# Kernel optimization log

Hardware: AMD Instinct MI355X
Metric: run time of the kernel (lower is better)

The kernel has to match this reference:

```python
import jax, jax.numpy as jnp
import numpy as np

B, S, H, I, E, TOP_K = 2, 2048, 1024, 2048, 8, 2


def setup_inputs() -> dict:
    key = jax.random.key(0)
    k1, k2, k3, k4, k5 = jax.random.split(key, 5)
    scale_h = 1.0 / np.sqrt(H)
    scale_i = 1.0 / np.sqrt(I)
    return {
        "hidden_states": jax.random.normal(k1, (B, S, H), dtype=jnp.float32),
        "router_w": jax.random.normal(k2, (H, E), dtype=jnp.float32) * scale_h,
        "gate_w": jax.random.normal(k3, (E, H, I), dtype=jnp.float32) * scale_h,
        "up_w": jax.random.normal(k4, (E, H, I), dtype=jnp.float32) * scale_h,
        "out_w": jax.random.normal(k5, (E, I, H), dtype=jnp.float32) * scale_i,
    }


def reference(hidden_states, router_w, gate_w, up_w, out_w):
    b, s, h = hidden_states.shape
    x = hidden_states.reshape(-1, h)  # [T, H], T = B*S

    # Router: logits -> softmax -> top-k -> renormalize -> dense routing matrix
    router_logits = x @ router_w  # [T, E]
    router_probs = jax.nn.softmax(router_logits, axis=-1)
    top_p, top_i = jax.lax.top_k(router_probs, TOP_K)  # [T, K]
    top_p = top_p / jnp.sum(top_p, axis=-1, keepdims=True)
    one_hot = jax.nn.one_hot(top_i, E, dtype=top_p.dtype)  # [T, K, E]
    routing_full = jnp.sum(one_hot * top_p[..., None], axis=1)  # [T, E]
    routing_full = routing_full.T  # [E, T]

    # Dense all-expert FFN (SwiGLU), as in the original batched einsum form
    gate = jnp.einsum("th,ehm->etm", x, gate_w)  # [E, T, I]
    gate = jax.nn.silu(gate)
    intermediate = jnp.einsum("th,ehm->etm", x, up_w)  # [E, T, I]
    hidden = intermediate * gate
    expert_out = jnp.einsum("eti,eih->eth", hidden, out_w)  # [E, T, H]

    # Weighted combine over experts
    out = jnp.sum(expert_out * routing_full[:, :, None], axis=0)  # [T, H]
    out = out.reshape(b, s, h)
    return out, router_logits
```

## Files before the change

### kernel.cpp

```cpp
#include <hip/hip_runtime.h>
#include <hip/hip_bf16.h>
#include <stdint.h>

#define TT 4096
#define HH 1024
#define II 2048
#define EE 8
#define RB 16
#define NRB (TT / RB)
#define CSTRIDE 32

typedef short bf16x8 __attribute__((ext_vector_type(8)));
typedef float f32x4 __attribute__((ext_vector_type(4)));

__device__ __forceinline__ unsigned short f2bf(float f) {
  unsigned u = __float_as_uint(f);
  u += 0x7FFF + ((u >> 16) & 1);
  return (unsigned short)(u >> 16);
}

__device__ __forceinline__ void gl_lds16(const void* g, void* l) {
  auto gp = reinterpret_cast<const __attribute__((address_space(1))) unsigned int*>(
      reinterpret_cast<uintptr_t>(g));
  auto lp = reinterpret_cast<__attribute__((address_space(3))) unsigned int*>(
      reinterpret_cast<uintptr_t>(l));
  __builtin_amdgcn_global_load_lds(gp, lp, 16, 0, 0);
}

__device__ __forceinline__ void transpose_tile_wide(const float* __restrict__ in,
                                                    unsigned short* __restrict__ out,
                                                    int M, int N, int mB, int nB,
                                                    unsigned int* tl, int tid) {
  union F4 { float4 v; float f[4]; };
  int n4 = tid & 31;
  int mph = tid >> 5;
  F4 a[4], bq[4];
  const float* base = in + (size_t)mB * N + nB + n4 * 4;
#pragma unroll
  for (int it = 0; it < 4; ++it) {
    const float* p = base + (size_t)(2 * (mph + it * 8)) * N;
    a[it].v = *(const float4*)p;
    bq[it].v = *(const float4*)(p + N);
  }
#pragma unroll
  for (int it = 0; it < 4; ++it) {
    int mp = mph + it * 8;
#pragma unroll
    for (int i = 0; i < 4; ++i) {
      int n = n4 * 4 + i;
      unsigned v = (unsigned)f2bf(a[it].f[i]) | ((unsigned)f2bf(bq[it].f[i]) << 16);
      tl[n * 32 + ((mp + (n >> 2) + (n & 3)) & 31)] = v;
    }
  }
  __syncthreads();
  int md = tid & 7;
  int nr = tid >> 3;
#pragma unroll
  for (int it = 0; it < 4; ++it) {
    int n = nr + it * 32;
    int rot = (n >> 2) + (n & 3);
    unsigned vv[4];
#pragma unroll
    for (int k = 0; k < 4; ++k)
      vv[k] = tl[n * 32 + ((md * 4 + k + rot) & 31)];
    *(uint4*)(out + (size_t)(nB + n) * M + mB + md * 8) = make_uint4(vv[0], vv[1], vv[2], vv[3]);
  }
}

__global__ __launch_bounds__(256, 4)
void front_kernel(const float* __restrict__ x, const float* __restrict__ rw,
                  const float* __restrict__ gw, const float* __restrict__ uw,
                  const float* __restrict__ ow,
                  float* __restrict__ logits_out, unsigned short* __restrict__ xb,
                  unsigned short* __restrict__ gwt, unsigned short* __restrict__ uwt,
                  unsigned short* __restrict__ owt,
                  int* __restrict__ gcnt, int2* __restrict__ ttop) {
  __shared__ unsigned int tl[4096];
  int b = blockIdx.x;
  int tid = threadIdx.x;

  if (b >= NRB) {
    int idx = b - NRB;
    int which = idx >> 11;
    int r = idx & 2047;
    int e = r >> 8;
    int tile = r & 255;
    if (which < 2) {
      int bx = tile & 15, by = tile >> 4;
      const float* in = (which ? uw : gw) + (size_t)e * HH * II;
      unsigned short* o = (which ? uwt : gwt) + (size_t)e * HH * II;
      transpose_tile_wide(in, o, HH, II, by * 64, bx * 128, tl, tid);
    } else {
      int bx = tile & 7, by = tile >> 3;
      transpose_tile_wide(ow + (size_t)e * II * HH, owt + (size_t)e * II * HH,
                          II, HH, by * 64, bx * 128, tl, tid);
    }
    return;
  }

  __shared__ int bcnt[EE];
  int wave = tid >> 6, lane = tid & 63;
  if (tid < EE) bcnt[tid] = 0;
  __syncthreads();
  int t0 = b * RB;

  for (int sub = 0; sub < RB / 4; ++sub) {
    int li = sub * 4 + wave;
    int t = t0 + li;
    float acc[EE];
#pragma unroll
    for (int e = 0; e < EE; ++e) acc[e] = 0.f;
#pragma unroll
    for (int j = 0; j < 4; ++j) {
      int h = j * 256 + lane * 4;
      union F4 { float4 v; float f[4]; } xv;
      xv.v = *(const float4*)(x + (size_t)t * HH + h);
      union { unsigned short s[4]; uint2 v; } pk;
#pragma unroll
      for (int i = 0; i < 4; ++i) pk.s[i] = f2bf(xv.f[i]);
      *(uint2*)(xb + (size_t)t * HH + h) = pk.v;
#pragma unroll
      for (int i = 0; i < 4; ++i) {
        const float4* r4 = (const float4*)(rw + (h + i) * EE);
        float4 r0 = r4[0], r1 = r4[1];
        float xs = xv.f[i];
        acc[0] += xs * r0.x; acc[1] += xs * r0.y; acc[2] += xs * r0.z; acc[3] += xs * r0.w;
        acc[4] += xs * r1.x; acc[5] += xs * r1.y; acc[6] += xs * r1.z; acc[7] += xs * r1.w;
      }
    }
#pragma unroll
    for (int e = 0; e < EE; ++e)
#pragma unroll
      for (int off = 32; off; off >>= 1) acc[e] += __shfl_down(acc[e], off);
    if (lane == 0) {
      float4* lo = (float4*)(logits_out + (size_t)t * EE);
      lo[0] = make_float4(acc[0], acc[1], acc[2], acc[3]);
      lo[1] = make_float4(acc[4], acc[5], acc[6], acc[7]);
      int e0 = 0; float b0 = acc[0];
#pragma unroll
      for (int e = 1; e < EE; ++e) if (acc[e] > b0) { b0 = acc[e]; e0 = e; }
      int e1 = -1; float b1 = -3.4e38f;
#pragma unroll
      for (int e = 0; e < EE; ++e) if (e != e0 && acc[e] > b1) { b1 = acc[e]; e1 = e; }
      float w0 = 1.f / (1.f + __expf(b1 - b0));
      int lp0 = atomicAdd(&bcnt[e0], 1);
      int lp1 = atomicAdd(&bcnt[e1], 1);
      ttop[t] = make_int2(e0 | (e1 << 3) | (lp0 << 6) | (lp1 << 11), __float_as_int(w0));
    }
  }
  __syncthreads();
  if (tid < EE) gcnt[b * EE + tid] = bcnt[tid];
}

__global__ void scatter_kernel(const int* __restrict__ gcnt, const int2* __restrict__ ttop,
                               int* __restrict__ cnt, int* __restrict__ list,
                               int* __restrict__ tslot, float2* __restrict__ tw) {
  __shared__ int raw[NRB * EE];
  __shared__ int base[NRB][EE];
  int tid = threadIdx.x;
  for (int i = tid; i < NRB * EE; i += 256) raw[i] = gcnt[i];
  __syncthreads();
  if (tid < EE) {
    int s = 0;
    for (int b = 0; b < NRB; ++b) { base[b][tid] = s; s += raw[b * EE + tid]; }
    if (blockIdx.x == 0) cnt[tid * CSTRIDE] = s;
  }
  __syncthreads();
  int t = blockIdx.x * 256 + tid;
  int2 ti = ttop[t];
  int v = ti.x;
  float w0 = __int_as_float(ti.y);
  int e0 = v & 7, e1 = (v >> 3) & 7, lp0 = (v >> 6) & 31, lp1 = (v >> 11) & 31;
  int b = t >> 4;
  int p0 = base[b][e0] + lp0;
  int p1 = base[b][e1] + lp1;
  list[e0 * TT + p0] = t;
  list[e1 * TT + p1] = t;
  tslot[t * 2]     = (e0 << 16) | p0;
  tslot[t * 2 + 1] = (e1 << 16) | p1;
  tw[t] = make_float2(w0, 1.f - w0);
}

__launch_bounds__(256, 3)
__global__ void gemm1_kernel(const unsigned short* __restrict__ xb,
                             const unsigned short* __restrict__ gwt,
                             const unsigned short* __restrict__ uwt,
                             unsigned short* __restrict__ hidden,
                             const int* __restrict__ cnt, const int* __restrict__ list) {
  __shared__ __align__(16) unsigned short smem[16384];
  __shared__ int stok[128];
  int tid = threadIdx.x;
  int e = blockIdx.z;

  int cn = cnt[e * CSTRIDE];
  int hb0 = 0;
  for (int i = 0; i < EE; ++i) hb0 += (i < e) ? cnt[i * CSTRIDE] : 0;
  int mBase = blockIdx.y * 128;
  if (mBase >= cn) return;
  int nBase = blockIdx.x * 64;

  int wave = tid >> 6, lane = tid & 63;
  if (tid < 128) {
    int g = mBase + tid;
    stok[tid] = list[e * TT + (g < cn ? g : cn - 1)];
  }
  __syncthreads();

  const char* gaddr[4];
  int lofs[4];
#pragma unroll
  for (int j = 0; j < 4; ++j) {
    int c = wave * 256 + j * 64 + lane;
    const char* g;
    if (c < 512) {
      int r = c >> 2, kc = (c & 3) ^ ((r >> 1) & 3);
      g = (const char*)xb + (size_t)stok[r] * (HH * 2) + kc * 16;
    } else if (c < 768) {
      int cc = c - 512, r = cc >> 2, kc = (cc & 3) ^ ((r >> 1) & 3);
      g = (const char*)gwt + ((size_t)e * II + nBase + r) * (HH * 2) + kc * 16;
    } else {
      int cc = c - 768, r = cc >> 2, kc = (cc & 3) ^ ((r >> 1) & 3);
      g = (const char*)uwt + ((size_t)e * II + nBase + r) * (HH * 2) + kc * 16;
    }
    gaddr[j] = g;
    lofs[j] = c * 16;
  }

  int q = lane >> 4, m16 = lane & 15;
  int wr = wave & 1, wc = wave >> 1;
  int faddrA[4], faddrBg[2], faddrBu[2];
#pragma unroll
  for (int mi = 0; mi < 4; ++mi) {
    int R = wr * 64 + mi * 16 + m16;
    faddrA[mi] = (R * 4 + (q ^ ((R >> 1) & 3))) * 16;
  }
#pragma unroll
  for (int ni = 0; ni < 2; ++ni) {
    int n = wc * 32 + ni * 16 + m16;
    faddrBg[ni] = (512 + n * 4 + (q ^ ((n >> 1) & 3))) * 16;
    faddrBu[ni] = (768 + n * 4 + (q ^ ((n >> 1) & 3))) * 16;
  }

  f32x4 zero4 = {0.f, 0.f, 0.f, 0.f};
  f32x4 accG[4][2], accU[4][2];
#pragma unroll
  for (int mi = 0; mi < 4; ++mi)
#pragma unroll
    for (int ni = 0; ni < 2; ++ni) { accG[mi][ni] = zero4; accU[mi][ni] = zero4; }

  char* smemc = (char*)smem;
#pragma unroll
  for (int j = 0; j < 4; ++j) {
    gl_lds16(gaddr[j], smemc + lofs[j]);
    gaddr[j] += 64;
  }
  __syncthreads();

  const int NK = HH / 32;
  for (int kt = 0; kt < NK; ++kt) {
    int cur = kt & 1;
    if (kt + 1 < NK) {
#pragma unroll
      for (int j = 0; j < 4; ++j) {
        gl_lds16(gaddr[j], smemc + (cur ^ 1) * 16384 + lofs[j]);
        gaddr[j] += 64;
      }
    }
    const char* sb = smemc + cur * 16384;
    bf16x8 aF[4], bG[2], bU[2];
#pragma unroll
    for (int mi = 0; mi < 4; ++mi) aF[mi] = *(const bf16x8*)(sb + faddrA[mi]);
#pragma unroll
    for (int ni = 0; ni < 2; ++ni) {
      bG[ni] = *(const bf16x8*)(sb + faddrBg[ni]);
      bU[ni] = *(const bf16x8*)(sb + faddrBu[ni]);
    }
#pragma unroll
    for (int mi = 0; mi < 4; ++mi)
#pragma unroll
      for (int ni = 0; ni < 2; ++ni) {
        accG[mi][ni] = __builtin_amdgcn_mfma_f32_16x16x32_bf16(aF[mi], bG[ni], accG[mi][ni], 0, 0, 0);
        accU[mi][ni] = __builtin_amdgcn_mfma_f32_16x16x32_bf16(aF[mi], bU[ni], accU[mi][ni], 0, 0, 0);
      }
    __syncthreads();
  }

  int hb = hb0 + mBase;
  int rowsValid = cn - mBase; if (rowsValid > 128) rowsValid = 128;
#pragma unroll
  for (int mi = 0; mi < 4; ++mi)
#pragma unroll
    for (int ni = 0; ni < 2; ++ni)
#pragma unroll
      for (int r = 0; r < 4; ++r) {
        int row = wr * 64 + mi * 16 + q * 4 + r;
        if (row < rowsValid) {
          float g = accG[mi][ni][r], u = accU[mi][ni][r];
          float h = g / (1.f + __expf(-g)) * u;
          hidden[(size_t)(hb + row) * II + nBase + wc * 32 + ni * 16 + m16] = f2bf(h);
        }
      }
}

__launch_bounds__(256, 3)
__global__ void gemm2_kernel(const unsigned short* __restrict__ hidden,
                             const unsigned short* __restrict__ owt,
                             float* __restrict__ expert_out,
                             const int* __restrict__ cnt) {
  int e = blockIdx.z;
  int cn = cnt[e * CSTRIDE];
  int hb0 = 0;
  for (int i = 0; i < EE; ++i) hb0 += (i < e) ? cnt[i * CSTRIDE] : 0;
  int mBase = blockIdx.y * 128;
  if (mBase >= cn) return;
  int nBase = blockIdx.x * 128;

  __shared__ __align__(16) unsigned short smem[16384];

  int tid = threadIdx.x, wave = tid >> 6, lane = tid & 63;
  int hb = hb0 + mBase;
  const char* gaddr[4];
  int lofs[4];
#pragma unroll
  for (int j = 0; j < 4; ++j) {
    int c = wave * 256 + j * 64 + lane;
    const char* g;
    if (c < 512) {
      int r = c >> 2, kc = (c & 3) ^ ((r >> 1) & 3);
      g = (const char*)hidden + (size_t)(hb + r) * (II * 2) + kc * 16;
    } else {
      int cc = c - 512, r = cc >> 2, kc = (cc & 3) ^ ((r >> 1) & 3);
      g = (const char*)owt + ((size_t)e * HH + nBase + r) * (II * 2) + kc * 16;
    }
    gaddr[j] = g;
    lofs[j] = c * 16;
  }

  int q = lane >> 4, m16 = lane & 15;
  int wr = wave & 1, wc = wave >> 1;
  int faddrA[4], faddrB[4];
#pragma unroll
  for (int mi = 0; mi < 4; ++mi) {
    int R = wr * 64 + mi * 16 + m16;
    faddrA[mi] = (R * 4 + (q ^ ((R >> 1) & 3))) * 16;
  }
#pragma unroll
  for (int ni = 0; ni < 4; ++ni) {
    int n = wc * 64 + ni * 16 + m16;
    faddrB[ni] = (512 + n * 4 + (q ^ ((n >> 1) & 3))) * 16;
  }

  f32x4 zero4 = {0.f, 0.f, 0.f, 0.f};
  f32x4 acc[4][4];
#pragma unroll
  for (int mi = 0; mi < 4; ++mi)
#pragma unroll
    for (int ni = 0; ni < 4; ++ni) acc[mi][ni] = zero4;

  char* smemc = (char*)smem;
#pragma unroll
  for (int j = 0; j < 4; ++j) {
    gl_lds16(gaddr[j], smemc + lofs[j]);
    gaddr[j] += 64;
  }
  __syncthreads();

  const int NK = II / 32;
  for (int kt = 0; kt < NK; ++kt) {
    int cur = kt & 1;
    if (kt + 1 < NK) {
#pragma unroll
      for (int j = 0; j < 4; ++j) {
        gl_lds16(gaddr[j], smemc + (cur ^ 1) * 16384 + lofs[j]);
        gaddr[j] += 64;
      }
    }
    const char* sb = smemc + cur * 16384;
    bf16x8 aF[4], bF[4];
#pragma unroll
    for (int mi = 0; mi < 4; ++mi) aF[mi] = *(const bf16x8*)(sb + faddrA[mi]);
#pragma unroll
    for (int ni = 0; ni < 4; ++ni) bF[ni] = *(const bf16x8*)(sb + faddrB[ni]);
#pragma unroll
    for (int mi = 0; mi < 4; ++mi)
#pragma unroll
      for (int ni = 0; ni < 4; ++ni)
        acc[mi][ni] = __builtin_amdgcn_mfma_f32_16x16x32_bf16(aF[mi], bF[ni], acc[mi][ni], 0, 0, 0);
    __syncthreads();
  }

  int rowsValid = cn - mBase; if (rowsValid > 128) rowsValid = 128;
#pragma unroll
  for (int mi = 0; mi < 4; ++mi)
#pragma unroll
    for (int ni = 0; ni < 4; ++ni)
#pragma unroll
      for (int r = 0; r < 4; ++r) {
        int row = wr * 64 + mi * 16 + q * 4 + r;
        if (row < rowsValid)
          expert_out[(size_t)(hb + row) * HH + nBase + wc * 64 + ni * 16 + m16] = acc[mi][ni][r];
      }
}

__global__ void combine_kernel(const float* __restrict__ expert_out,
                               const int* __restrict__ cnt, const int* __restrict__ tslot,
                               const float2* __restrict__ tw, float* __restrict__ out) {
  int pre[EE];
  int s = 0;
#pragma unroll
  for (int e = 0; e < EE; ++e) { pre[e] = s; s += cnt[e * CSTRIDE]; }
  int t = blockIdx.x;
  int s0 = tslot[t * 2], s1 = tslot[t * 2 + 1];
  float2 w = tw[t];
  int r0 = pre[s0 >> 16] + (s0 & 0xFFFF);
  int r1 = pre[s1 >> 16] + (s1 & 0xFFFF);
  const float4* a = (const float4*)(expert_out + (size_t)r0 * HH);
  const float4* b = (const float4*)(expert_out + (size_t)r1 * HH);
  float4* o = (float4*)(out + (size_t)t * HH);
  int c = threadIdx.x;
  float4 av = a[c], bv = b[c];
  o[c] = make_float4(w.x * av.x + w.y * bv.x, w.x * av.y + w.y * bv.y,
                     w.x * av.z + w.y * bv.z, w.x * av.w + w.y * bv.w);
}

extern "C" void kernel_launch(void* const* d_in, const int* in_sizes, int n_in,
                              void* d_out, int out_size, void* d_ws, size_t ws_size,
                              hipStream_t stream) {
  (void)in_sizes; (void)n_in; (void)out_size; (void)ws_size;
  const float* x  = (const float*)d_in[0];
  const float* rw = (const float*)d_in[1];
  const float* gw = (const float*)d_in[2];
  const float* uw = (const float*)d_in[3];
  const float* ow = (const float*)d_in[4];
  float* out = (float*)d_out;
  float* logits = out + (size_t)TT * HH;

  char* ws = (char*)d_ws;
  size_t o = 0;
  auto alloc = [&](size_t bytes) {
    char* p = ws + o;
    o += (bytes + 255) & ~(size_t)255;
    return p;
  };
  unsigned short* xb  = (unsigned short*)alloc((size_t)TT * HH * 2);
  unsigned short* gwt = (unsigned short*)alloc((size_t)EE * II * HH * 2);
  unsigned short* uwt = (unsigned short*)alloc((size_t)EE * II * HH * 2);
  unsigned short* owt = (unsigned short*)alloc((size_t)EE * HH * II * 2);
  unsigned short* hidden = (unsigned short*)alloc((size_t)(2 * TT + 128) * II * 2);
  int*    cnt   = (int*)alloc(EE * CSTRIDE * 4);
  int*    list  = (int*)alloc((size_t)EE * TT * 4);
  int*    tslot = (int*)alloc((size_t)TT * 2 * 4);
  float2* tw    = (float2*)alloc((size_t)TT * 8);
  int*    gcnt  = (int*)alloc((size_t)NRB * EE * 4);
  int2*   ttop  = (int2*)alloc((size_t)TT * 8);
  float* expert_out = (float*)gwt;

  front_kernel<<<NRB + 3 * 2048, 256, 0, stream>>>(x, rw, gw, uw, ow, logits, xb, gwt, uwt, owt,
                                                   gcnt, ttop);
  scatter_kernel<<<TT / 256, 256, 0, stream>>>(gcnt, ttop, cnt, list, tslot, tw);
  gemm1_kernel<<<dim3(32, 32, EE), 256, 0, stream>>>(xb, gwt, uwt, hidden, cnt, list);
  gemm2_kernel<<<dim3(HH / 128, TT / 128, EE), 256, 0, stream>>>(hidden, owt, expert_out, cnt);
  combine_kernel<<<TT, 256, 0, stream>>>(expert_out, cnt, tslot, tw, out);
}
```

Measured before the change: 419.3 us.

## Fuse weighted expert combine into gemm2 epilogue via atomic scatter-add

Removes the combine kernel and the fp32 expert_out intermediate. gemm2 now looks up each row's token index and routing weight and atomically adds the weighted result straight into the output. The output is zeroed by extra blocks appended to front_kernel. Launch-bound occupancy hints are also raised for front, gemm1 and gemm2. This trades a global write plus re-read of expert outputs for float atomics, which contend only lightly since each token gets two contributions, and makes summation order nondeterministic.

```diff
diff --git a/kernel.cpp b/kernel.cpp
--- a/kernel.cpp
+++ b/kernel.cpp
@@ -9,6 +9,8 @@
 #define RB 16
 #define NRB (TT / RB)
 #define CSTRIDE 32
+#define NTRB (3 * 2048)
+#define NZB 256
 
 typedef short bf16x8 __attribute__((ext_vector_type(8)));
 typedef float f32x4 __attribute__((ext_vector_type(4)));
@@ -67,17 +69,27 @@
   }
 }
 
-__global__ __launch_bounds__(256, 4)
+__global__ __launch_bounds__(256, 8)
 void front_kernel(const float* __restrict__ x, const float* __restrict__ rw,
                   const float* __restrict__ gw, const float* __restrict__ uw,
                   const float* __restrict__ ow,
                   float* __restrict__ logits_out, unsigned short* __restrict__ xb,
                   unsigned short* __restrict__ gwt, unsigned short* __restrict__ uwt,
                   unsigned short* __restrict__ owt,
-                  int* __restrict__ gcnt, int2* __restrict__ ttop) {
+                  int* __restrict__ gcnt, int2* __restrict__ ttop,
+                  float* __restrict__ outz) {
   __shared__ unsigned int tl[4096];
   int b = blockIdx.x;
   int tid = threadIdx.x;
+
+  if (b >= NRB + NTRB) {
+    int zb = b - NRB - NTRB;
+    float4* o = (float4*)outz + (size_t)zb * 4096 + tid;
+    float4 z = make_float4(0.f, 0.f, 0.f, 0.f);
+#pragma unroll
+    for (int k = 0; k < 16; ++k) o[k * 256] = z;
+    return;
+  }
 
   if (b >= NRB) {
     int idx = b - NRB;
@@ -154,7 +166,7 @@
 
 __global__ void scatter_kernel(const int* __restrict__ gcnt, const int2* __restrict__ ttop,
                                int* __restrict__ cnt, int* __restrict__ list,
-                               int* __restrict__ tslot, float2* __restrict__ tw) {
+                               float* __restrict__ rwt) {
   __shared__ int raw[NRB * EE];
   __shared__ int base[NRB][EE];
   int tid = threadIdx.x;
@@ -176,12 +188,11 @@
   int p1 = base[b][e1] + lp1;
   list[e0 * TT + p0] = t;
   list[e1 * TT + p1] = t;
-  tslot[t * 2]     = (e0 << 16) | p0;
-  tslot[t * 2 + 1] = (e1 << 16) | p1;
-  tw[t] = make_float2(w0, 1.f - w0);
-}
-
-__launch_bounds__(256, 3)
+  rwt[e0 * TT + p0] = w0;
+  rwt[e1 * TT + p1] = 1.f - w0;
+}
+
+__launch_bounds__(256, 4)
 __global__ void gemm1_kernel(const unsigned short* __restrict__ xb,
                              const unsigned short* __restrict__ gwt,
                              const unsigned short* __restrict__ uwt,
@@ -302,11 +313,12 @@
       }
 }
 
-__launch_bounds__(256, 3)
+__launch_bounds__(256, 4)
 __global__ void gemm2_kernel(const unsigned short* __restrict__ hidden,
                              const unsigned short* __restrict__ owt,
-                             float* __restrict__ expert_out,
-                             const int* __restrict__ cnt) {
+                             float* __restrict__ out,
+                             const int* __restrict__ cnt, const int* __restrict__ list,
+                             const float* __restrict__ rwt) {
   int e = blockIdx.z;
   int cn = cnt[e * CSTRIDE];
   int hb0 = 0;
@@ -316,9 +328,17 @@
   int nBase = blockIdx.x * 128;
 
   __shared__ __align__(16) unsigned short smem[16384];
+  __shared__ int stok[128];
+  __shared__ float swt[128];
 
   int tid = threadIdx.x, wave = tid >> 6, lane = tid & 63;
   int hb = hb0 + mBase;
+  if (tid < 128) {
+    int g = mBase + tid;
+    int gi = g < cn ? g : cn - 1;
+    stok[tid] = list[e * TT + gi];
+    swt[tid] = rwt[e * TT + gi];
+  }
   const char* gaddr[4];
   int lofs[4];
 #pragma unroll
@@ -393,34 +413,17 @@
 #pragma unroll
   for (int mi = 0; mi < 4; ++mi)
 #pragma unroll
-    for (int ni = 0; ni < 4; ++ni)
-#pragma unroll
-      for (int r = 0; r < 4; ++r) {
-        int row = wr * 64 + mi * 16 + q * 4 + r;
-        if (row < rowsValid)
-          expert_out[(size_t)(hb + row) * HH + nBase + wc * 64 + ni * 16 + m16] = acc[mi][ni][r];
-      }
-}
-
-__global__ void combine_kernel(const float* __restrict__ expert_out,
-                               const int* __restrict__ cnt, const int* __restrict__ tslot,
-                               const float2* __restrict__ tw, float* __restrict__ out) {
-  int pre[EE];
-  int s = 0;
-#pragma unroll
-  for (int e = 0; e < EE; ++e) { pre[e] = s; s += cnt[e * CSTRIDE]; }
-  int t = blockIdx.x;
-  int s0 = tslot[t * 2], s1 = tslot[t * 2 + 1];
-  float2 w = tw[t];
-  int r0 = pre[s0 >> 16] + (s0 & 0xFFFF);
-  int r1 = pre[s1 >> 16] + (s1 & 0xFFFF);
-  const float4* a = (const float4*)(expert_out + (size_t)r0 * HH);
-  const float4* b = (const float4*)(expert_out + (size_t)r1 * HH);
-  float4* o = (float4*)(out + (size_t)t * HH);
-  int c = threadIdx.x;
-  float4 av = a[c], bv = b[c];
-  o[c] = make_float4(w.x * av.x + w.y * bv.x, w.x * av.y + w.y * bv.y,
-                     w.x * av.z + w.y * bv.z, w.x * av.w + w.y * bv.w);
+    for (int r = 0; r < 4; ++r) {
+      int row = wr * 64 + mi * 16 + q * 4 + r;
+      if (row < rowsValid) {
+        int t = stok[row];
+        float w = swt[row];
+        float* orow = out + (size_t)t * HH + nBase + wc * 64 + m16;
+#pragma unroll
+        for (int ni = 0; ni < 4; ++ni)
+          atomicAdd(orow + ni * 16, w * acc[mi][ni][r]);
+      }
+    }
 }
 
 extern "C" void kernel_launch(void* const* d_in, const int* in_sizes, int n_in,
@@ -449,16 +452,13 @@
   unsigned short* hidden = (unsigned short*)alloc((size_t)(2 * TT + 128) * II * 2);
   int*    cnt   = (int*)alloc(EE * CSTRIDE * 4);
   int*    list  = (int*)alloc((size_t)EE * TT * 4);
-  int*    tslot = (int*)alloc((size_t)TT * 2 * 4);
-  float2* tw    = (float2*)alloc((size_t)TT * 8);
+  float*  rwt   = (float*)alloc((size_t)EE * TT * 4);
   int*    gcnt  = (int*)alloc((size_t)NRB * EE * 4);
   int2*   ttop  = (int2*)alloc((size_t)TT * 8);
-  float* expert_out = (float*)gwt;
-
-  front_kernel<<<NRB + 3 * 2048, 256, 0, stream>>>(x, rw, gw, uw, ow, logits, xb, gwt, uwt, owt,
-                                                   gcnt, ttop);
-  scatter_kernel<<<TT / 256, 256, 0, stream>>>(gcnt, ttop, cnt, list, tslot, tw);
+
+  front_kernel<<<NRB + NTRB + NZB, 256, 0, stream>>>(x, rw, gw, uw, ow, logits, xb, gwt, uwt, owt,
+                                                     gcnt, ttop, out);
+  scatter_kernel<<<TT / 256, 256, 0, stream>>>(gcnt, ttop, cnt, list, rwt);
   gemm1_kernel<<<dim3(32, 32, EE), 256, 0, stream>>>(xb, gwt, uwt, hidden, cnt, list);
-  gemm2_kernel<<<dim3(HH / 128, TT / 128, EE), 256, 0, stream>>>(hidden, owt, expert_out, cnt);
-  combine_kernel<<<TT, 256, 0, stream>>>(expert_out, cnt, tslot, tw, out);
-}
+  gemm2_kernel<<<dim3(HH / 128, TT / 128, EE), 256, 0, stream>>>(hidden, owt, out, cnt, list, rwt);
+}
```

Result: slower. 448.7 us (+7.0%).
